# Performance work log

Measured on AMD Instinct MI355X. Metric: run time of the kernel, lower is better.

The kernel has to match this reference:

```python
import jax, jax.numpy as jnp
import numpy as np

N = 4096          # num_nodes
E = 65536         # num edges (avg degree 16)
WALK_LENGTH = 16
OUT_DIM = 8


def setup_inputs() -> dict:
    key = jax.random.key(0)
    k1, k2 = jax.random.split(key, 2)
    edge_index = jax.random.randint(k1, (2, E), 0, N, dtype=jnp.int64)
    # nn.Linear(walk_length, out_dim): weight [out_dim, walk_length], bias [out_dim]
    linear_w = (jax.random.normal(k2, (OUT_DIM, WALK_LENGTH), jnp.float32)
                / np.float32(np.sqrt(WALK_LENGTH)))
    linear_b = jnp.zeros((OUT_DIM,), jnp.float32)
    return {"edge_index": edge_index, "num_nodes": N,
            "linear_w": linear_w, "linear_b": linear_b}


def reference(edge_index, num_nodes, linear_w, linear_b):
    row, col = edge_index[0], edge_index[1]
    # out-degree via scatter_add, clamped to >= 1
    deg = jnp.zeros((num_nodes,), jnp.float32).at[row].add(1.0)
    deg = jnp.maximum(deg, 1.0)
    rw_values = 1.0 / deg[row]                              # [E]
    # random-walk transition matrix P[row, col] = 1/deg[row]
    # (.at[].add sums duplicate edges, matching coalesce())
    P = jnp.zeros((num_nodes, num_nodes), jnp.float32).at[row, col].add(rw_values)
    Pt = P.T

    def step(cur, _):
        cur = Pt @ cur                                      # [N, N]
        return cur, jnp.diagonal(cur)                       # k-step return probs

    cur0 = jnp.eye(num_nodes, dtype=jnp.float32)
    _, diags = jax.lax.scan(step, cur0, None, length=WALK_LENGTH)
    rw_diag = diags.T                                       # [N, walk_length]
    return rw_diag @ linear_w.T + linear_b                  # [N, out_dim]
```

## Files before the change

### kernel.cpp

```cpp
#include <hip/hip_runtime.h>
#include <hip/hip_fp16.h>
#include <hip/hip_fp8.h>

#define NNODES 4096
#define LWALK 16
#define ODIM 8

#define FP8_SCALE 256.0f
#define FP8_INV   0.00390625f
#define FP8_INV2  1.52587890625e-05f

typedef unsigned int uint4n __attribute__((ext_vector_type(4)));
typedef unsigned int uint2n __attribute__((ext_vector_type(2)));
typedef float float2n __attribute__((ext_vector_type(2)));

__device__ __forceinline__ void dec8f(unsigned int lo, unsigned int hi, float* f) {
#if __has_builtin(__builtin_amdgcn_cvt_pk_f32_fp8)
    float2n p;
    p = __builtin_amdgcn_cvt_pk_f32_fp8((int)lo, false); f[0] = p.x; f[1] = p.y;
    p = __builtin_amdgcn_cvt_pk_f32_fp8((int)lo, true);  f[2] = p.x; f[3] = p.y;
    p = __builtin_amdgcn_cvt_pk_f32_fp8((int)hi, false); f[4] = p.x; f[5] = p.y;
    p = __builtin_amdgcn_cvt_pk_f32_fp8((int)hi, true);  f[6] = p.x; f[7] = p.y;
#else
    unsigned int w[2] = {lo, hi};
    const unsigned char* b = (const unsigned char*)w;
#pragma unroll
    for (int i = 0; i < 8; ++i) {
        __hip_fp8_e4m3 t; t.__x = b[i]; f[i] = (float)t;
    }
#endif
}

__device__ __forceinline__ void enc8f(const float* a, unsigned int* lo,
                                      unsigned int* hi) {
#if __has_builtin(__builtin_amdgcn_cvt_pk_fp8_f32)
    int l = 0, h = 0;
    l = __builtin_amdgcn_cvt_pk_fp8_f32(a[0], a[1], l, false);
    l = __builtin_amdgcn_cvt_pk_fp8_f32(a[2], a[3], l, true);
    h = __builtin_amdgcn_cvt_pk_fp8_f32(a[4], a[5], h, false);
    h = __builtin_amdgcn_cvt_pk_fp8_f32(a[6], a[7], h, true);
    *lo = (unsigned int)l; *hi = (unsigned int)h;
#else
    unsigned char b[8];
#pragma unroll
    for (int i = 0; i < 8; ++i)
        b[i] = __hip_cvt_float_to_fp8(a[i], __HIP_SATFINITE, __HIP_E4M3);
    unsigned int w[2];
    __builtin_memcpy(w, b, 8);
    *lo = w[0]; *hi = w[1];
#endif
}

__device__ __forceinline__ void dec16f(uint4n w, float* f) {
    dec8f(w.x, w.y, f);
    dec8f(w.z, w.w, f + 8);
}

__device__ __forceinline__ uint4n enc16f(const float* a) {
    uint4n o;
    unsigned int lo, hi;
    enc8f(a, &lo, &hi);     o.x = lo; o.y = hi;
    enc8f(a + 8, &lo, &hi); o.z = lo; o.w = hi;
    return o;
}

__global__ void detect_fmt_k(const void* ei, int E, int* flag) {
    if (blockIdx.x == 0 && threadIdx.x == 0) {
        const long long* p = (const long long*)ei;
        int ok = 1;
        for (int i = 0; i < 64; ++i) {
            long long v = p[i];
            if (v < 0 || v >= NNODES) { ok = 0; break; }
        }
        *flag = ok;
    }
}

__device__ __forceinline__ int load_idx(const void* p, int i, int fmt) {
    if (fmt) return (int)((const long long*)p)[i];
    return ((const int*)p)[i];
}

__global__ void build_deg_cnt_k(const void* ei, int E, int* deg, int* cnt,
                                const int* fmt) {
    int e = blockIdx.x * blockDim.x + threadIdx.x;
    if (e >= E) return;
    int f = *fmt;
    int r = load_idx(ei, e, f);
    int c = load_idx(ei, E + e, f);
    atomicAdd(&deg[r], 1);
    atomicAdd(&cnt[c], 1);
}

__global__ void scan_k(const int* __restrict__ cnt, int* __restrict__ rowptr,
                       int* __restrict__ cursor) {
    __shared__ int sm[1024];
    int tid = threadIdx.x;
    int v0 = (cnt[4 * tid + 0] + 7) & ~7;
    int v1 = (cnt[4 * tid + 1] + 7) & ~7;
    int v2 = (cnt[4 * tid + 2] + 7) & ~7;
    int v3 = (cnt[4 * tid + 3] + 7) & ~7;
    int tsum = v0 + v1 + v2 + v3;
    sm[tid] = tsum;
    __syncthreads();
    int val = tsum;
    for (int off = 1; off < 1024; off <<= 1) {
        int t = (tid >= off) ? sm[tid - off] : 0;
        __syncthreads();
        val += t;
        sm[tid] = val;
        __syncthreads();
    }
    int excl = val - tsum;
    int p0 = excl, p1 = excl + v0, p2 = p1 + v1, p3 = p2 + v2;
    rowptr[4 * tid + 0] = p0; rowptr[4 * tid + 1] = p1;
    rowptr[4 * tid + 2] = p2; rowptr[4 * tid + 3] = p3;
    cursor[4 * tid + 0] = p0; cursor[4 * tid + 1] = p1;
    cursor[4 * tid + 2] = p2; cursor[4 * tid + 3] = p3;
    if (tid == 1023) rowptr[4096] = val;
}

__global__ void fill_csr_k(const void* ei, int E, const int* __restrict__ deg,
                           int* cursor, uint2* __restrict__ epad, const int* fmt) {
    int e = blockIdx.x * blockDim.x + threadIdx.x;
    if (e >= E) return;
    int f = *fmt;
    int r = load_idx(ei, e, f);
    int c = load_idx(ei, E + e, f);
    int pos = atomicAdd(&cursor[c], 1);
    int d = deg[r];
    float v = 1.0f / (float)(d < 1 ? 1 : d);
    epad[pos] = make_uint2((unsigned)r, __float_as_uint(v));
}

__global__ void pad_fill_k(const int* __restrict__ rowptr,
                           const int* __restrict__ cursor,
                           uint2* __restrict__ epad) {
    int c = blockIdx.x * blockDim.x + threadIdx.x;
    if (c >= NNODES) return;
    for (int p = cursor[c]; p < rowptr[c + 1]; ++p)
        epad[p] = make_uint2(0u, 0u);
}

__global__ __launch_bounds__(256) void x2build_k(
    const int* __restrict__ rowptr, const uint2* __restrict__ epad,
    unsigned char* __restrict__ Y8, float* __restrict__ rw) {
    __shared__ float row[NNODES];
    __shared__ float dia1;
    const int c = blockIdx.x;
    const int t = threadIdx.x;
    for (int i = t; i < NNODES; i += 256) row[i] = 0.f;
    if (t == 0) dia1 = 0.f;
    __syncthreads();
    const int beg = rowptr[c], end = rowptr[c + 1];
    for (int i1 = beg + t; i1 < end; i1 += 256) {
        uint2 e1 = epad[i1];
        float v = __uint_as_float(e1.y);
        if (v != 0.f) {
            int r = (int)e1.x;
            if (r == c) atomicAdd(&dia1, v);
            int b2 = rowptr[r], n2 = rowptr[r + 1];
            for (int j = b2; j < n2; ++j) {
                uint2 e2 = epad[j];
                float w = __uint_as_float(e2.y);
                if (w != 0.f) atomicAdd(&row[e2.x], v * w);
            }
        }
    }
    __syncthreads();
    if (t == 0) {
        rw[c * LWALK + 0] = dia1;
        rw[c * LWALK + 1] = row[c];
    }
    float f[16];
    const int base = t * 16;
#pragma unroll
    for (int u = 0; u < 16; ++u) f[u] = row[base + u] * FP8_SCALE;
    uint4n o = enc16f(f);
    __builtin_nontemporal_store(o, (uint4n*)(Y8 + (size_t)c * NNODES + base));
}

__global__ __launch_bounds__(256) void fused8_k(
    const unsigned char* __restrict__ X8, unsigned char* __restrict__ Y8,
    const int* __restrict__ rowptr, const uint2* __restrict__ epad,
    float* __restrict__ rw, int kcol,
    const unsigned char* __restrict__ PA, const unsigned char* __restrict__ PB,
    int colO, int colE, int nspmm) {
    __shared__ __half bt[64][66];
    __shared__ __half ct[64][66];
    const int bid = blockIdx.x;
    if (bid < nspmm) {
        const int slab = bid & 3;
        const int lane = threadIdx.x & 63;
        const int c =
            __builtin_amdgcn_readfirstlane((bid >> 2) * 4 + (threadIdx.x >> 6));
        const int colo = slab * 1024 + lane * 16;
        const unsigned char* Xs = X8 + colo;
        const int beg = rowptr[c], end = rowptr[c + 1];
        float a[16];
#pragma unroll
        for (int u = 0; u < 16; ++u) a[u] = 0.f;
        for (int e = beg; e < end; e += 8) {
            uint2 ed[8];
#pragma unroll
            for (int j = 0; j < 8; ++j) ed[j] = epad[e + j];
            uint4n x[8];
#pragma unroll
            for (int j = 0; j < 8; ++j)
                x[j] = *(const uint4n*)(Xs + (size_t)ed[j].x * NNODES);
#pragma unroll
            for (int j = 0; j < 8; ++j) {
                float v = __uint_as_float(ed[j].y);
                float f[16];
                dec16f(x[j], f);
#pragma unroll
                for (int u = 0; u < 16; ++u) a[u] = fmaf(f[u], v, a[u]);
            }
        }
        if ((c >> 10) == slab && lane == ((c & 1023) >> 4)) {
            float d = 0.f;
#pragma unroll
            for (int u = 0; u < 16; ++u)
                if ((c & 15) == u) d = a[u];
            rw[c * LWALK + kcol] = d * FP8_INV;
        }
        uint4n o = enc16f(a);
        __builtin_nontemporal_store(o, (uint4n*)(Y8 + (size_t)c * NNODES + colo));
    } else {
        const int pb = bid - nspmm;
        const int i0 = (pb & 63) * 64;
        const int Jbeg = (pb >> 6) * (NNODES / 16);
        const int Jend = Jbeg + (NNODES / 16);
        const int t = threadIdx.x;
        const int li = t >> 2;
        const int q = t & 3;
        const int c0 = q * 16;
        float accO = 0.f, accE = 0.f;
        for (int J = Jbeg; J < Jend; J += 64) {
            uint4n b16 = __builtin_nontemporal_load(
                (const uint4n*)(PB + (size_t)(J + li) * NNODES + i0 + c0));
            uint4n g16 = __builtin_nontemporal_load(
                (const uint4n*)(PA + (size_t)(J + li) * NNODES + i0 + c0));
            __syncthreads();
            float bf[16], gf[16];
            dec16f(b16, bf);
            dec16f(g16, gf);
#pragma unroll
            for (int s = 0; s < 16; ++s) {
                bt[c0 + s][li] = __float2half(bf[s]);
                ct[c0 + s][li] = __float2half(gf[s]);
            }
            __syncthreads();
            uint4n a16 = __builtin_nontemporal_load(
                (const uint4n*)(PA + (size_t)(i0 + li) * NNODES + J + c0));
            float af[16];
            dec16f(a16, af);
#pragma unroll
            for (int s = 0; s < 16; ++s) {
                accO = fmaf(af[s], __half2float(bt[li][c0 + s]), accO);
                accE = fmaf(af[s], __half2float(ct[li][c0 + s]), accE);
            }
        }
        accO += __shfl_xor(accO, 1);
        accO += __shfl_xor(accO, 2);
        accE += __shfl_xor(accE, 1);
        accE += __shfl_xor(accE, 2);
        if (q == 0) {
            atomicAdd(&rw[(i0 + li) * LWALK + colO], accO * FP8_INV2);
            atomicAdd(&rw[(i0 + li) * LWALK + colE], accE * FP8_INV2);
        }
    }
}

__global__ void linear_k(const float* __restrict__ rw, const float* __restrict__ W,
                         const float* __restrict__ b, float* __restrict__ out) {
    int i = blockIdx.x * blockDim.x + threadIdx.x;
    if (i >= NNODES * ODIM) return;
    int s = i >> 3, d = i & 7;
    float acc = b[d];
#pragma unroll
    for (int k = 0; k < LWALK; ++k)
        acc = fmaf(rw[s * LWALK + k], W[d * LWALK + k], acc);
    out[i] = acc;
}

extern "C" void kernel_launch(void* const* d_in, const int* in_sizes, int n_in,
                              void* d_out, int out_size, void* d_ws, size_t ws_size,
                              hipStream_t stream) {
    const void* ei = d_in[0];
    int E = in_sizes[0] / 2;
    const float* W = (const float*)d_in[2];
    const float* bias = (const float*)d_in[3];
    float* out = (float*)d_out;

    char* ws = (char*)d_ws;
    size_t off = 0;
    auto alloc = [&](size_t bytes) -> char* {
        char* p = ws + off;
        off = (off + bytes + 255) & ~(size_t)255;
        return p;
    };
    int* flag = (int*)alloc(4);
    int* deg = (int*)alloc(NNODES * 4);
    int* cnt = (int*)alloc(NNODES * 4);
    int* rowptr = (int*)alloc((NNODES + 1) * 4);
    int* cursor = (int*)alloc(NNODES * 4);
    uint2* epad = (uint2*)alloc(((size_t)E + 8 * NNODES) * 8);
    float* rw = (float*)alloc(NNODES * LWALK * 4);
    unsigned char* A = (unsigned char*)alloc((size_t)NNODES * NNODES);
    unsigned char* B = (unsigned char*)alloc((size_t)NNODES * NNODES);
    unsigned char* C = (unsigned char*)alloc((size_t)NNODES * NNODES);

    (void)hipMemsetAsync(deg, 0, NNODES * 4, stream);
    (void)hipMemsetAsync(cnt, 0, NNODES * 4, stream);
    (void)hipMemsetAsync(rw, 0, NNODES * LWALK * 4, stream);
    detect_fmt_k<<<1, 64, 0, stream>>>(ei, E, flag);
    build_deg_cnt_k<<<(E + 255) / 256, 256, 0, stream>>>(ei, E, deg, cnt, flag);
    scan_k<<<1, 1024, 0, stream>>>(cnt, rowptr, cursor);
    fill_csr_k<<<(E + 255) / 256, 256, 0, stream>>>(ei, E, deg, cursor, epad, flag);
    pad_fill_k<<<(NNODES + 255) / 256, 256, 0, stream>>>(rowptr, cursor, epad);

    x2build_k<<<NNODES, 256, 0, stream>>>(rowptr, epad, A, rw);

    const int SG = 4096;
    fused8_k<<<SG, 256, 0, stream>>>(A, B, rowptr, epad, rw, 2, nullptr, nullptr, 0, 0, SG);
    fused8_k<<<SG, 256, 0, stream>>>(B, C, rowptr, epad, rw, 3, nullptr, nullptr, 0, 0, SG);
    fused8_k<<<SG, 256, 0, stream>>>(C, A, rowptr, epad, rw, 4, nullptr, nullptr, 0, 0, SG);
    fused8_k<<<SG + 1024, 256, 0, stream>>>(A, B, rowptr, epad, rw, 5, A, C, 8, 9, SG);
    fused8_k<<<SG + 1024, 256, 0, stream>>>(B, C, rowptr, epad, rw, 6, B, A, 10, 11, SG);
    fused8_k<<<SG + 1024, 256, 0, stream>>>(C, A, rowptr, epad, rw, 7, C, B, 12, 13, SG);
    fused8_k<<<1024, 256, 0, stream>>>(nullptr, nullptr, rowptr, epad, rw, 0, A, C, 14, 15, 0);

    linear_k<<<(NNODES * ODIM + 255) / 256, 256, 0, stream>>>(rw, W, bias, out);
}
```

Measured before the change: 304.8 us.

## Shrink CSR padding to 4, parallelize x2build per neighbor row, dedicate finale kernel

Row padding in the CSR drops from multiples of 8 to multiples of 4, and the SpMM inner loop batch shrinks to match. The aim is to waste less work on zero padding edges, at the cost of less memory-level parallelism per iteration. The x2build kernel now splits threads into 16 groups, with each group's 16 lanes cooperatively walking the second-hop neighbor list; this balances work across threads. The last diagonal-only pass moves into a separate finale_k kernel, and fill_csr_k is renamed with an empty extra branch.

Measured after the change: 295.3 us. 3.1% less time.

```diff
diff --git a/kernel.cpp b/kernel.cpp
--- a/kernel.cpp
+++ b/kernel.cpp
@@ -96,10 +96,10 @@
                        int* __restrict__ cursor) {
     __shared__ int sm[1024];
     int tid = threadIdx.x;
-    int v0 = (cnt[4 * tid + 0] + 7) & ~7;
-    int v1 = (cnt[4 * tid + 1] + 7) & ~7;
-    int v2 = (cnt[4 * tid + 2] + 7) & ~7;
-    int v3 = (cnt[4 * tid + 3] + 7) & ~7;
+    int v0 = (cnt[4 * tid + 0] + 3) & ~3;
+    int v1 = (cnt[4 * tid + 1] + 3) & ~3;
+    int v2 = (cnt[4 * tid + 2] + 3) & ~3;
+    int v3 = (cnt[4 * tid + 3] + 3) & ~3;
     int tsum = v0 + v1 + v2 + v3;
     sm[tid] = tsum;
     __syncthreads();
@@ -120,17 +120,20 @@
     if (tid == 1023) rowptr[4096] = val;
 }
 
-__global__ void fill_csr_k(const void* ei, int E, const int* __restrict__ deg,
-                           int* cursor, uint2* __restrict__ epad, const int* fmt) {
+__global__ void fill_pad_k(const void* ei, int E, const int* __restrict__ deg,
+                           int* cursor, const int* __restrict__ rowptr,
+                           uint2* __restrict__ epad, const int* fmt) {
     int e = blockIdx.x * blockDim.x + threadIdx.x;
-    if (e >= E) return;
-    int f = *fmt;
-    int r = load_idx(ei, e, f);
-    int c = load_idx(ei, E + e, f);
-    int pos = atomicAdd(&cursor[c], 1);
-    int d = deg[r];
-    float v = 1.0f / (float)(d < 1 ? 1 : d);
-    epad[pos] = make_uint2((unsigned)r, __float_as_uint(v));
+    if (e < E) {
+        int f = *fmt;
+        int r = load_idx(ei, e, f);
+        int c = load_idx(ei, E + e, f);
+        int pos = atomicAdd(&cursor[c], 1);
+        int d = deg[r];
+        float v = 1.0f / (float)(d < 1 ? 1 : d);
+        epad[pos] = make_uint2((unsigned)r, __float_as_uint(v));
+    } else if (e < E + NNODES) {
+    }
 }
 
 __global__ void pad_fill_k(const int* __restrict__ rowptr,
@@ -153,14 +156,16 @@
     if (t == 0) dia1 = 0.f;
     __syncthreads();
     const int beg = rowptr[c], end = rowptr[c + 1];
-    for (int i1 = beg + t; i1 < end; i1 += 256) {
+    const int g = t >> 4;
+    const int l = t & 15;
+    for (int i1 = beg + g; i1 < end; i1 += 16) {
         uint2 e1 = epad[i1];
         float v = __uint_as_float(e1.y);
         if (v != 0.f) {
             int r = (int)e1.x;
-            if (r == c) atomicAdd(&dia1, v);
+            if (r == c && l == 0) atomicAdd(&dia1, v);
             int b2 = rowptr[r], n2 = rowptr[r + 1];
-            for (int j = b2; j < n2; ++j) {
+            for (int j = b2 + l; j < n2; j += 16) {
                 uint2 e2 = epad[j];
                 float w = __uint_as_float(e2.y);
                 if (w != 0.f) atomicAdd(&row[e2.x], v * w);
@@ -200,16 +205,16 @@
         float a[16];
 #pragma unroll
         for (int u = 0; u < 16; ++u) a[u] = 0.f;
-        for (int e = beg; e < end; e += 8) {
-            uint2 ed[8];
-#pragma unroll
-            for (int j = 0; j < 8; ++j) ed[j] = epad[e + j];
-            uint4n x[8];
-#pragma unroll
-            for (int j = 0; j < 8; ++j)
+        for (int e = beg; e < end; e += 4) {
+            uint2 ed[4];
+#pragma unroll
+            for (int j = 0; j < 4; ++j) ed[j] = epad[e + j];
+            uint4n x[4];
+#pragma unroll
+            for (int j = 0; j < 4; ++j)
                 x[j] = *(const uint4n*)(Xs + (size_t)ed[j].x * NNODES);
 #pragma unroll
-            for (int j = 0; j < 8; ++j) {
+            for (int j = 0; j < 4; ++j) {
                 float v = __uint_as_float(ed[j].y);
                 float f[16];
                 dec16f(x[j], f);
@@ -272,6 +277,59 @@
     }
 }
 
+__global__ __launch_bounds__(256) void finale_k(
+    const unsigned char* __restrict__ PA, const unsigned char* __restrict__ PB,
+    float* __restrict__ rw, const float* __restrict__ W,
+    const float* __restrict__ b, float* __restrict__ out, int npair) {
+    __shared__ __half bt[64][66];
+    __shared__ __half ct[64][66];
+    const int bid = blockIdx.x;
+    if (bid < npair) {
+        const int pb = bid;
+        const int i0 = (pb & 63) * 64;
+        const int Jbeg = (pb >> 6) * (NNODES / 16);
+        const int Jend = Jbeg + (NNODES / 16);
+        const int t = threadIdx.x;
+        const int li = t >> 2;
+        const int q = t & 3;
+        const int c0 = q * 16;
+        float accO = 0.f, accE = 0.f;
+        for (int J = Jbeg; J < Jend; J += 64) {
+            uint4n b16 = __builtin_nontemporal_load(
+                (const uint4n*)(PB + (size_t)(J + li) * NNODES + i0 + c0));
+            uint4n g16 = __builtin_nontemporal_load(
+                (const uint4n*)(PA + (size_t)(J + li) * NNODES + i0 + c0));
+            __syncthreads();
+            float bf[16], gf[16];
+            dec16f(b16, bf);
+            dec16f(g16, gf);
+#pragma unroll
+            for (int s = 0; s < 16; ++s) {
+                bt[c0 + s][li] = __float2half(bf[s]);
+                ct[c0 + s][li] = __float2half(gf[s]);
+            }
+            __syncthreads();
+            uint4n a16 = __builtin_nontemporal_load(
+                (const uint4n*)(PA + (size_t)(i0 + li) * NNODES + J + c0));
+            float af[16];
+            dec16f(a16, af);
+#pragma unroll
+            for (int s = 0; s < 16; ++s) {
+                accO = fmaf(af[s], __half2float(bt[li][c0 + s]), accO);
+                accE = fmaf(af[s], __half2float(ct[li][c0 + s]), accE);
+            }
+        }
+        accO += __shfl_xor(accO, 1);
+        accO += __shfl_xor(accO, 2);
+        accE += __shfl_xor(accE, 1);
+        accE += __shfl_xor(accE, 2);
+        if (q == 0) {
+            atomicAdd(&rw[(i0 + li) * LWALK + 14], accO * FP8_INV2);
+            atomicAdd(&rw[(i0 + li) * LWALK + 15], accE * FP8_INV2);
+        }
+    }
+}
+
 __global__ void linear_k(const float* __restrict__ rw, const float* __restrict__ W,
                          const float* __restrict__ b, float* __restrict__ out) {
     int i = blockIdx.x * blockDim.x + threadIdx.x;
@@ -305,7 +363,7 @@
     int* cnt = (int*)alloc(NNODES * 4);
     int* rowptr = (int*)alloc((NNODES + 1) * 4);
     int* cursor = (int*)alloc(NNODES * 4);
-    uint2* epad = (uint2*)alloc(((size_t)E + 8 * NNODES) * 8);
+    uint2* epad = (uint2*)alloc(((size_t)E + 4 * NNODES) * 8);
     float* rw = (float*)alloc(NNODES * LWALK * 4);
     unsigned char* A = (unsigned char*)alloc((size_t)NNODES * NNODES);
     unsigned char* B = (unsigned char*)alloc((size_t)NNODES * NNODES);
@@ -317,7 +375,8 @@
     detect_fmt_k<<<1, 64, 0, stream>>>(ei, E, flag);
     build_deg_cnt_k<<<(E + 255) / 256, 256, 0, stream>>>(ei, E, deg, cnt, flag);
     scan_k<<<1, 1024, 0, stream>>>(cnt, rowptr, cursor);
-    fill_csr_k<<<(E + 255) / 256, 256, 0, stream>>>(ei, E, deg, cursor, epad, flag);
+    fill_pad_k<<<(E + 255) / 256, 256, 0, stream>>>(ei, E, deg, cursor, rowptr,
+                                                    epad, flag);
     pad_fill_k<<<(NNODES + 255) / 256, 256, 0, stream>>>(rowptr, cursor, epad);
 
     x2build_k<<<NNODES, 256, 0, stream>>>(rowptr, epad, A, rw);
@@ -329,7 +388,8 @@
     fused8_k<<<SG + 1024, 256, 0, stream>>>(A, B, rowptr, epad, rw, 5, A, C, 8, 9, SG);
     fused8_k<<<SG + 1024, 256, 0, stream>>>(B, C, rowptr, epad, rw, 6, B, A, 10, 11, SG);
     fused8_k<<<SG + 1024, 256, 0, stream>>>(C, A, rowptr, epad, rw, 7, C, B, 12, 13, SG);
-    fused8_k<<<1024, 256, 0, stream>>>(nullptr, nullptr, rowptr, epad, rw, 0, A, C, 14, 15, 0);
-
+    finale_k<<<1024, 256, 0, stream>>>(A, C, rw, W, bias, out, 1024);
     linear_k<<<(NNODES * ODIM + 255) / 256, 256, 0, stream>>>(rw, W, bias, out);
-}
+
+    (void)fill_pad_k;
+}
```
